# Performance work log

Measured on AMD Instinct MI355X. Metric: run time of the kernel, lower is better.

## Reference

```python
import jax, jax.numpy as jnp
import numpy as np

B, C_ENT, C_REL = 32768, 1000, 500


def setup_inputs() -> dict:
    key = jax.random.key(0)
    ks = jax.random.split(key, 6)
    return {
        "sub_input": jax.random.normal(ks[0], (B, C_ENT), dtype=jnp.float32),
        "relation_input": jax.random.normal(ks[1], (B, C_REL), dtype=jnp.float32),
        "obj_input": jax.random.normal(ks[2], (B, C_ENT), dtype=jnp.float32),
        "sub_target": jax.random.randint(ks[3], (B,), 0, C_ENT, dtype=jnp.int32),
        "relation_target": jax.random.randint(ks[4], (B,), 0, C_REL, dtype=jnp.int32),
        "obj_target": jax.random.randint(ks[5], (B,), 0, C_ENT, dtype=jnp.int32),
    }


def reference(sub_input, relation_input, obj_input, sub_target, relation_target, obj_target):
    s = jax.nn.softmax(sub_input, axis=1)
    r = jax.nn.softmax(relation_input, axis=1)
    o = jax.nn.softmax(obj_input, axis=1)
    b = s.shape[0]
    rows = jnp.arange(b)

    # ground-truth triplet probability
    gt = s[rows, sub_target] * r[rows, relation_target] * o[rows, obj_target]

    # top-2 values/indices per row (replaces full torch.sort)
    sv, si = jax.lax.top_k(s, 2)
    rv, ri = jax.lax.top_k(r, 2)
    ov, oi = jax.lax.top_k(o, 2)

    # all three argmaxes match the targets?
    cond = (si[:, 0] == sub_target) & (ri[:, 0] == relation_target) & (oi[:, 0] == obj_target)

    # 8 combinations of top-2 probs; second-smallest of the 8 (torch.sort ascending, index 1)
    tmp = (sv[:, :, None, None] * rv[:, None, :, None] * ov[:, None, None, :]).reshape(b, 8)
    second_smallest = jnp.sort(tmp, axis=1)[:, 1]

    top1 = sv[:, 0] * rv[:, 0] * ov[:, 0]
    pre = jnp.where(cond, second_smallest, top1)

    out = 1.0 - gt + pre
    return jnp.mean(jnp.maximum(out, 0.0))
```

## Files before the change

### kernel.cpp

```cpp
#include <hip/hip_runtime.h>
#include <float.h>
#include <limits.h>


constexpr int B      = 32768;
constexpr int C_ENT  = 1000;
constexpr int C_REL  = 500;


template<int NK>
__device__ inline void lane_top2(const float4* v, float& m1, float& m2) {
  float hi[2 * NK], lo[2 * NK];
#pragma unroll
  for (int k = 0; k < NK; ++k) {
    hi[2 * k]     = fmaxf(v[k].x, v[k].y);
    lo[2 * k]     = fminf(v[k].x, v[k].y);
    hi[2 * k + 1] = fmaxf(v[k].z, v[k].w);
    lo[2 * k + 1] = fminf(v[k].z, v[k].w);
  }
#pragma unroll
  for (int half = NK; half >= 1; half >>= 1) {
#pragma unroll
    for (int i = 0; i < half; ++i) {
      const float ha = hi[i], hb = hi[i + half];
      const float la = lo[i], lb = lo[i + half];
      hi[i] = fmaxf(ha, hb);
      lo[i] = fmaxf(fmaxf(la, lb), fminf(ha, hb));
    }
  }
  m1 = hi[0];
  m2 = lo[0];
}

template<int NK>
__device__ inline void lane_z_idx(const float4* v, int lane, float m1, float& z, int& idx) {
  float zp[NK];
  idx = INT_MAX;
#pragma unroll
  for (int k = 0; k < NK; ++k) {
    const int base = 4 * (lane + 64 * k);
    const float a0 = v[k].x, a1 = v[k].y, a2 = v[k].z, a3 = v[k].w;
    zp[k] = (__expf(a0 - m1) + __expf(a1 - m1)) + (__expf(a2 - m1) + __expf(a3 - m1));
    const int i01 = min(a0 == m1 ? base     : INT_MAX, a1 == m1 ? base + 1 : INT_MAX);
    const int i23 = min(a2 == m1 ? base + 2 : INT_MAX, a3 == m1 ? base + 3 : INT_MAX);
    idx = min(idx, min(i01, i23));
  }
  if constexpr (NK == 4) z = (zp[0] + zp[1]) + (zp[2] + zp[3]);
  else                   z = zp[0] + zp[1];
}

template<int NK, int C4>
__device__ inline void wave_stats2(const float* __restrict__ rowA,
                                   const float* __restrict__ rowB,
                                   int lane, int tA, int tB,
                                   float4* __restrict__ outp) {
  const float4* a4 = (const float4*)rowA;
  const float4* b4 = (const float4*)rowB;
  float4 va[NK], vb[NK];
#pragma unroll
  for (int k = 0; k < NK - 1; ++k) {
    va[k] = a4[lane + 64 * k];
    vb[k] = b4[lane + 64 * k];
  }
  {
    const int  i  = lane + 64 * (NK - 1);
    const bool ok = (i < C4);
    const int  ic = ok ? i : (C4 - 1);
    float4 ta = a4[ic], tb = b4[ic];
    ta.x = ok ? ta.x : -FLT_MAX;  ta.y = ok ? ta.y : -FLT_MAX;
    ta.z = ok ? ta.z : -FLT_MAX;  ta.w = ok ? ta.w : -FLT_MAX;
    tb.x = ok ? tb.x : -FLT_MAX;  tb.y = ok ? tb.y : -FLT_MAX;
    tb.z = ok ? tb.z : -FLT_MAX;  tb.w = ok ? tb.w : -FLT_MAX;
    va[NK - 1] = ta;
    vb[NK - 1] = tb;
  }
  const float xa = rowA[tA];
  const float xb = rowB[tB];

  float m1a, m2a, m1b, m2b;
  lane_top2<NK>(va, m1a, m2a);
  lane_top2<NK>(vb, m1b, m2b);

#pragma unroll
  for (int off = 32; off; off >>= 1) {
    const float p1a = __shfl_xor(m1a, off), p2a = __shfl_xor(m2a, off);
    const float p1b = __shfl_xor(m1b, off), p2b = __shfl_xor(m2b, off);
    m2a = fmaxf(fmaxf(m2a, p2a), fminf(m1a, p1a));
    m1a = fmaxf(m1a, p1a);
    m2b = fmaxf(fmaxf(m2b, p2b), fminf(m1b, p1b));
    m1b = fmaxf(m1b, p1b);
  }

  float za, zb;
  int   ia, ib;
  lane_z_idx<NK>(va, lane, m1a, za, ia);
  lane_z_idx<NK>(vb, lane, m1b, zb, ib);

#pragma unroll
  for (int off = 32; off; off >>= 1) {
    za += __shfl_xor(za, off);
    zb += __shfl_xor(zb, off);
    ia  = min(ia, __shfl_xor(ia, off));
    ib  = min(ib, __shfl_xor(ib, off));
  }

  if (lane == 0) {
    const float iZa = 1.0f / za;
    const float iZb = 1.0f / zb;
    outp[0] = make_float4(iZa, __expf(m2a - m1a) * iZa, __expf(xa - m1a) * iZa,
                          __int_as_float(ia));
    outp[1] = make_float4(iZb, __expf(m2b - m1b) * iZb, __expf(xb - m1b) * iZb,
                          __int_as_float(ib));
  }
}

__global__ __launch_bounds__(256) void stats2_kernel(
    const float* __restrict__ s, const float* __restrict__ r, const float* __restrict__ o,
    const int* __restrict__ st, const int* __restrict__ rt, const int* __restrict__ ot,
    float4* __restrict__ out4) {
  const int wid  = threadIdx.x >> 6;
  const int lane = threadIdx.x & 63;
  const int gw   = blockIdx.x * 4 + wid;
  const int m    = gw >> 14;
  const int p    = gw & 16383;
  const int row  = 2 * p;
  if (m == 0)
    wave_stats2<4, C_ENT / 4>(s + (size_t)row * C_ENT, s + (size_t)(row + 1) * C_ENT,
                              lane, st[row], st[row + 1], out4 + row);
  else if (m == 1)
    wave_stats2<4, C_ENT / 4>(o + (size_t)row * C_ENT, o + (size_t)(row + 1) * C_ENT,
                              lane, ot[row], ot[row + 1], out4 + B + row);
  else
    wave_stats2<2, C_REL / 4>(r + (size_t)row * C_REL, r + (size_t)(row + 1) * C_REL,
                              lane, rt[row], rt[row + 1], out4 + 2 * B + row);
}

__global__ __launch_bounds__(256) void combine_kernel(
    const float4* __restrict__ stat4,
    const int* __restrict__ st, const int* __restrict__ rt, const int* __restrict__ ot,
    float* __restrict__ partial) {
  const int row = blockIdx.x * 256 + threadIdx.x;
  const float4 S = stat4[row];
  const float4 O = stat4[B + row];
  const float4 R = stat4[2 * B + row];
  const float gt   = S.z * R.z * O.z;
  const float top1 = S.x * R.x * O.x;
  const float c1 = S.x * R.y * O.y;
  const float c2 = S.y * R.x * O.y;
  const float c3 = S.y * R.y * O.x;
  const float second = fminf(c1, fminf(c2, c3));
  const bool cond = (__float_as_int(S.w) == st[row]) &&
                    (__float_as_int(R.w) == rt[row]) &&
                    (__float_as_int(O.w) == ot[row]);
  const float pre = cond ? second : top1;
  partial[row] = fmaxf(1.0f - gt + pre, 0.0f);
}


__device__ inline void combine_stats(float& m1, int& i1, float& m2, float& Z,
                                     float bm1, int bi1, float bm2, float bZ) {
  bool bwin = (bm1 > m1) || (bm1 == m1 && bi1 < i1);
  float wm1 = bwin ? bm1 : m1;
  int   wi1 = bwin ? bi1 : i1;
  float wm2 = bwin ? bm2 : m2;
  float lm1 = bwin ? m1  : bm1;
  float wZ  = bwin ? bZ  : Z;
  float lZ  = bwin ? Z   : bZ;
  m1 = wm1; i1 = wi1;
  m2 = fmaxf(wm2, lm1);
  Z  = wZ + lZ * __expf(lm1 - wm1);
}

template<int NK, int C4>
__device__ inline void row_stats(const float* __restrict__ row, int lane, int target,
                                 float& p_top1, float& p_top2, int& amax, float& p_tgt) {
  const float4* row4 = (const float4*)row;
  float4 v[NK];
#pragma unroll
  for (int k = 0; k < NK; ++k) {
    int idx = lane + 64 * k;
    v[k] = (idx < C4) ? row4[idx] : make_float4(-FLT_MAX, -FLT_MAX, -FLT_MAX, -FLT_MAX);
  }
  float m1 = -FLT_MAX, m2 = -FLT_MAX;
  int   i1 = 0x7fffffff;
#pragma unroll
  for (int k = 0; k < NK; ++k) {
    int base = 4 * (lane + 64 * k);
    float a0 = v[k].x, a1 = v[k].y, a2 = v[k].z, a3 = v[k].w;
    if (a0 > m1) { m2 = m1; m1 = a0; i1 = base;     } else if (a0 > m2) m2 = a0;
    if (a1 > m1) { m2 = m1; m1 = a1; i1 = base + 1; } else if (a1 > m2) m2 = a1;
    if (a2 > m1) { m2 = m1; m1 = a2; i1 = base + 2; } else if (a2 > m2) m2 = a2;
    if (a3 > m1) { m2 = m1; m1 = a3; i1 = base + 3; } else if (a3 > m2) m2 = a3;
  }
  float Z = 0.f;
#pragma unroll
  for (int k = 0; k < NK; ++k) {
    Z += __expf(v[k].x - m1); Z += __expf(v[k].y - m1);
    Z += __expf(v[k].z - m1); Z += __expf(v[k].w - m1);
  }
#pragma unroll
  for (int off = 32; off > 0; off >>= 1) {
    float bm1 = __shfl_xor(m1, off);
    int   bi1 = __shfl_xor(i1, off);
    float bm2 = __shfl_xor(m2, off);
    float bZ  = __shfl_xor(Z,  off);
    combine_stats(m1, i1, m2, Z, bm1, bi1, bm2, bZ);
  }
  float invZ = 1.0f / Z;
  float xt   = row[target];
  p_top1 = invZ;
  p_top2 = __expf(m2 - m1) * invZ;
  p_tgt  = __expf(xt - m1) * invZ;
  amax   = i1;
}

template<bool ATOMIC>
__global__ __launch_bounds__(256) void rank_loss_kernel(
    const float* __restrict__ s, const float* __restrict__ r, const float* __restrict__ o,
    const int* __restrict__ st, const int* __restrict__ rt, const int* __restrict__ ot,
    float* __restrict__ partial, float* __restrict__ out) {
  const int wid  = threadIdx.x >> 6;
  const int lane = threadIdx.x & 63;
  const int row  = blockIdx.x * 4 + wid;

  const float* srow = s + (size_t)row * C_ENT;
  const float* rrow = r + (size_t)row * C_REL;
  const float* orow = o + (size_t)row * C_ENT;
  const int tS = st[row], tR = rt[row], tO = ot[row];

  float sp0, sp1, spt; int sa;
  float rp0, rp1, rpt; int ra;
  float op0, op1, opt; int oa;
  row_stats<4, C_ENT / 4>(srow, lane, tS, sp0, sp1, sa, spt);
  row_stats<2, C_REL / 4>(rrow, lane, tR, rp0, rp1, ra, rpt);
  row_stats<4, C_ENT / 4>(orow, lane, tO, op0, op1, oa, opt);

  if (lane == 0) {
    float gt   = spt * rpt * opt;
    float top1 = sp0 * rp0 * op0;
    float c1 = sp0 * rp1 * op1;
    float c2 = sp1 * rp0 * op1;
    float c3 = sp1 * rp1 * op0;
    float second = fminf(c1, fminf(c2, c3));
    bool cond = (sa == tS) && (ra == tR) && (oa == tO);
    float pre = cond ? second : top1;
    float val = fmaxf(1.0f - gt + pre, 0.0f);
    if (ATOMIC) atomicAdd(out, val * (1.0f / (float)B));
    else        partial[row] = val;
  }
}


__global__ __launch_bounds__(1024) void reduce_sum_kernel(const float* __restrict__ p,
                                                          float* __restrict__ out) {
  const float4* p4 = (const float4*)p;
  float sum = 0.f;
  for (int i = threadIdx.x; i < B / 4; i += 1024) {
    float4 v = p4[i];
    sum += (v.x + v.y) + (v.z + v.w);
  }
#pragma unroll
  for (int off = 32; off > 0; off >>= 1) sum += __shfl_xor(sum, off);
  __shared__ float lds[16];
  if ((threadIdx.x & 63) == 0) lds[threadIdx.x >> 6] = sum;
  __syncthreads();
  if (threadIdx.x == 0) {
    float t = 0.f;
#pragma unroll
    for (int i = 0; i < 16; ++i) t += lds[i];
    out[0] = t * (1.0f / (float)B);
  }
}

extern "C" void kernel_launch(void* const* d_in, const int* in_sizes, int n_in,
                              void* d_out, int out_size, void* d_ws, size_t ws_size,
                              hipStream_t stream) {
  const float* s  = (const float*)d_in[0];
  const float* r  = (const float*)d_in[1];
  const float* o  = (const float*)d_in[2];
  const int*   st = (const int*)d_in[3];
  const int*   rt = (const int*)d_in[4];
  const int*   ot = (const int*)d_in[5];
  float* out = (float*)d_out;

  const size_t statBytes = (size_t)3 * B * sizeof(float4);
  if (ws_size >= statBytes + (size_t)B * sizeof(float)) {
    float4* stat4  = (float4*)d_ws;
    float* partial = (float*)((char*)d_ws + statBytes);
    stats2_kernel<<<3 * B / 8, 256, 0, stream>>>(s, r, o, st, rt, ot, stat4);
    combine_kernel<<<B / 256, 256, 0, stream>>>(stat4, st, rt, ot, partial);
    reduce_sum_kernel<<<1, 1024, 0, stream>>>(partial, out);
  } else if (ws_size >= (size_t)B * sizeof(float)) {
    float* partial = (float*)d_ws;
    rank_loss_kernel<false><<<B / 4, 256, 0, stream>>>(s, r, o, st, rt, ot, partial, nullptr);
    reduce_sum_kernel<<<1, 1024, 0, stream>>>(partial, out);
  } else {
    hipMemsetAsync(d_out, 0, sizeof(float), stream);
    rank_loss_kernel<true><<<B / 4, 256, 0, stream>>>(s, r, o, st, rt, ot, nullptr, out);
  }
}
```

Before: 320.1 us.

## Fuse stats, combine and reduce into one cooperative persistent kernel with DPP reductions

Replaces the three-kernel pipeline (stats, combine, reduce) with a single cooperative persistent kernel. Waves loop over row-pair units, then a grid sync is followed by per-block loss partial sums and a second grid sync for the final reduction. Wave-level shuffle reductions in the stats path are also replaced with DPP row/bank broadcast reductions that end in lane 63. The aim is to remove two launch gaps and the per-row partial write and read, and to make the cross-lane reductions cheaper. In exchange it adds grid-wide sync cost and limits the grid to resident blocks, which could reduce latency hiding for the memory-bound stats phase.

```diff
diff --git a/kernel.cpp b/kernel.cpp
--- a/kernel.cpp
+++ b/kernel.cpp
@@ -1,11 +1,63 @@
 #include <hip/hip_runtime.h>
+#include <hip/hip_cooperative_groups.h>
 #include <float.h>
 #include <limits.h>
+
+namespace cg = cooperative_groups;
 
 
 constexpr int B      = 32768;
 constexpr int C_ENT  = 1000;
 constexpr int C_REL  = 500;
+constexpr int NUNITS = 3 * B / 2;
+
+
+template<int CTRL, int RM>
+__device__ inline float fdpp(float x, float ident) {
+  return __int_as_float(__builtin_amdgcn_update_dpp(
+      __float_as_int(ident), __float_as_int(x), CTRL, RM, 0xF, false));
+}
+template<int CTRL, int RM>
+__device__ inline int idpp(int x, int ident) {
+  return __builtin_amdgcn_update_dpp(ident, x, CTRL, RM, 0xF, false);
+}
+__device__ inline float readlane63(float x) {
+  return __int_as_float(__builtin_amdgcn_readlane(__float_as_int(x), 63));
+}
+
+template<int CTRL, int RM>
+__device__ inline void top2_stage(float& m1, float& m2) {
+  const float q1 = fdpp<CTRL, RM>(m1, -FLT_MAX);
+  const float q2 = fdpp<CTRL, RM>(m2, -FLT_MAX);
+  m2 = fmaxf(fmaxf(m2, q2), fminf(m1, q1));
+  m1 = fmaxf(m1, q1);
+}
+__device__ inline void top2_reduce63(float& m1, float& m2) {
+  top2_stage<0xB1,  0xF>(m1, m2);
+  top2_stage<0x4E,  0xF>(m1, m2);
+  top2_stage<0x141, 0xF>(m1, m2);
+  top2_stage<0x140, 0xF>(m1, m2);
+  top2_stage<0x142, 0xA>(m1, m2);
+  top2_stage<0x143, 0xC>(m1, m2);
+}
+__device__ inline float sum_reduce63(float z) {
+  z += fdpp<0xB1,  0xF>(z, 0.f);
+  z += fdpp<0x4E,  0xF>(z, 0.f);
+  z += fdpp<0x141, 0xF>(z, 0.f);
+  z += fdpp<0x140, 0xF>(z, 0.f);
+  z += fdpp<0x142, 0xA>(z, 0.f);
+  z += fdpp<0x143, 0xC>(z, 0.f);
+  return z;
+}
+__device__ inline int min_reduce63(int v) {
+  v = min(v, idpp<0xB1,  0xF>(v, INT_MAX));
+  v = min(v, idpp<0x4E,  0xF>(v, INT_MAX));
+  v = min(v, idpp<0x141, 0xF>(v, INT_MAX));
+  v = min(v, idpp<0x140, 0xF>(v, INT_MAX));
+  v = min(v, idpp<0x142, 0xA>(v, INT_MAX));
+  v = min(v, idpp<0x143, 0xC>(v, INT_MAX));
+  return v;
+}
 
 
 template<int NK>
@@ -80,31 +132,21 @@
   float m1a, m2a, m1b, m2b;
   lane_top2<NK>(va, m1a, m2a);
   lane_top2<NK>(vb, m1b, m2b);
-
-#pragma unroll
-  for (int off = 32; off; off >>= 1) {
-    const float p1a = __shfl_xor(m1a, off), p2a = __shfl_xor(m2a, off);
-    const float p1b = __shfl_xor(m1b, off), p2b = __shfl_xor(m2b, off);
-    m2a = fmaxf(fmaxf(m2a, p2a), fminf(m1a, p1a));
-    m1a = fmaxf(m1a, p1a);
-    m2b = fmaxf(fmaxf(m2b, p2b), fminf(m1b, p1b));
-    m1b = fmaxf(m1b, p1b);
-  }
+  top2_reduce63(m1a, m2a);
+  top2_reduce63(m1b, m2b);
+  m1a = readlane63(m1a);  m2a = readlane63(m2a);
+  m1b = readlane63(m1b);  m2b = readlane63(m2b);
 
   float za, zb;
   int   ia, ib;
   lane_z_idx<NK>(va, lane, m1a, za, ia);
   lane_z_idx<NK>(vb, lane, m1b, zb, ib);
-
-#pragma unroll
-  for (int off = 32; off; off >>= 1) {
-    za += __shfl_xor(za, off);
-    zb += __shfl_xor(zb, off);
-    ia  = min(ia, __shfl_xor(ia, off));
-    ib  = min(ib, __shfl_xor(ib, off));
-  }
-
-  if (lane == 0) {
+  za = sum_reduce63(za);
+  zb = sum_reduce63(zb);
+  ia = min_reduce63(ia);
+  ib = min_reduce63(ib);
+
+  if (lane == 63) {
     const float iZa = 1.0f / za;
     const float iZb = 1.0f / zb;
     outp[0] = make_float4(iZa, __expf(m2a - m1a) * iZa, __expf(xa - m1a) * iZa,
@@ -114,32 +156,25 @@
   }
 }
 
-__global__ __launch_bounds__(256) void stats2_kernel(
+__device__ inline void do_unit(int gw,
     const float* __restrict__ s, const float* __restrict__ r, const float* __restrict__ o,
     const int* __restrict__ st, const int* __restrict__ rt, const int* __restrict__ ot,
-    float4* __restrict__ out4) {
-  const int wid  = threadIdx.x >> 6;
-  const int lane = threadIdx.x & 63;
-  const int gw   = blockIdx.x * 4 + wid;
-  const int m    = gw >> 14;
-  const int p    = gw & 16383;
-  const int row  = 2 * p;
+    float4* __restrict__ stat4, int lane) {
+  const int m   = gw >> 14;
+  const int row = (gw & 16383) * 2;
   if (m == 0)
     wave_stats2<4, C_ENT / 4>(s + (size_t)row * C_ENT, s + (size_t)(row + 1) * C_ENT,
-                              lane, st[row], st[row + 1], out4 + row);
+                              lane, st[row], st[row + 1], stat4 + row);
   else if (m == 1)
     wave_stats2<4, C_ENT / 4>(o + (size_t)row * C_ENT, o + (size_t)(row + 1) * C_ENT,
-                              lane, ot[row], ot[row + 1], out4 + B + row);
+                              lane, ot[row], ot[row + 1], stat4 + B + row);
   else
     wave_stats2<2, C_REL / 4>(r + (size_t)row * C_REL, r + (size_t)(row + 1) * C_REL,
-                              lane, rt[row], rt[row + 1], out4 + 2 * B + row);
-}
-
-__global__ __launch_bounds__(256) void combine_kernel(
-    const float4* __restrict__ stat4,
-    const int* __restrict__ st, const int* __restrict__ rt, const int* __restrict__ ot,
-    float* __restrict__ partial) {
-  const int row = blockIdx.x * 256 + threadIdx.x;
+                              lane, rt[row], rt[row + 1], stat4 + 2 * B + row);
+}
+
+__device__ inline float row_loss(const float4* __restrict__ stat4, int row,
+                                 int ts, int tr, int to) {
   const float4 S = stat4[row];
   const float4 O = stat4[B + row];
   const float4 R = stat4[2 * B + row];
@@ -149,11 +184,87 @@
   const float c2 = S.y * R.x * O.y;
   const float c3 = S.y * R.y * O.x;
   const float second = fminf(c1, fminf(c2, c3));
-  const bool cond = (__float_as_int(S.w) == st[row]) &&
-                    (__float_as_int(R.w) == rt[row]) &&
-                    (__float_as_int(O.w) == ot[row]);
+  const bool cond = (__float_as_int(S.w) == ts) &&
+                    (__float_as_int(R.w) == tr) &&
+                    (__float_as_int(O.w) == to);
   const float pre = cond ? second : top1;
-  partial[row] = fmaxf(1.0f - gt + pre, 0.0f);
+  return fmaxf(1.0f - gt + pre, 0.0f);
+}
+
+
+__global__ __launch_bounds__(256, 8) void fused_kernel(
+    const float* __restrict__ s, const float* __restrict__ r, const float* __restrict__ o,
+    const int* __restrict__ st, const int* __restrict__ rt, const int* __restrict__ ot,
+    float4* __restrict__ stat4, float* __restrict__ partial, float* __restrict__ out) {
+  const int wid  = threadIdx.x >> 6;
+  const int lane = threadIdx.x & 63;
+  const int nslots = gridDim.x * 4;
+  for (int gw = blockIdx.x * 4 + wid; gw < NUNITS; gw += nslots)
+    do_unit(gw, s, r, o, st, rt, ot, stat4, lane);
+
+  cg::this_grid().sync();
+
+  float sum = 0.f;
+  for (int row = blockIdx.x * 256 + threadIdx.x; row < B; row += gridDim.x * 256)
+    sum += row_loss(stat4, row, st[row], rt[row], ot[row]);
+#pragma unroll
+  for (int off = 32; off; off >>= 1) sum += __shfl_xor(sum, off);
+  __shared__ float lds[4];
+  if (lane == 0) lds[wid] = sum;
+  __syncthreads();
+  if (threadIdx.x == 0) partial[blockIdx.x] = (lds[0] + lds[1]) + (lds[2] + lds[3]);
+
+  cg::this_grid().sync();
+
+  if (blockIdx.x == 0) {
+    float t = 0.f;
+    for (int i = threadIdx.x; i < (int)gridDim.x; i += 256) t += partial[i];
+#pragma unroll
+    for (int off = 32; off; off >>= 1) t += __shfl_xor(t, off);
+    if (lane == 0) lds[wid] = t;
+    __syncthreads();
+    if (threadIdx.x == 0)
+      out[0] = ((lds[0] + lds[1]) + (lds[2] + lds[3])) * (1.0f / (float)B);
+  }
+}
+
+
+__global__ __launch_bounds__(256) void stats2_kernel(
+    const float* __restrict__ s, const float* __restrict__ r, const float* __restrict__ o,
+    const int* __restrict__ st, const int* __restrict__ rt, const int* __restrict__ ot,
+    float4* __restrict__ out4) {
+  const int wid  = threadIdx.x >> 6;
+  const int lane = threadIdx.x & 63;
+  do_unit(blockIdx.x * 4 + wid, s, r, o, st, rt, ot, out4, lane);
+}
+
+__global__ __launch_bounds__(256) void combine_kernel(
+    const float4* __restrict__ stat4,
+    const int* __restrict__ st, const int* __restrict__ rt, const int* __restrict__ ot,
+    float* __restrict__ partial) {
+  const int row = blockIdx.x * 256 + threadIdx.x;
+  partial[row] = row_loss(stat4, row, st[row], rt[row], ot[row]);
+}
+
+__global__ __launch_bounds__(1024) void reduce_sum_kernel(const float* __restrict__ p,
+                                                          float* __restrict__ out) {
+  const float4* p4 = (const float4*)p;
+  float sum = 0.f;
+  for (int i = threadIdx.x; i < B / 4; i += 1024) {
+    float4 v = p4[i];
+    sum += (v.x + v.y) + (v.z + v.w);
+  }
+#pragma unroll
+  for (int off = 32; off > 0; off >>= 1) sum += __shfl_xor(sum, off);
+  __shared__ float lds[16];
+  if ((threadIdx.x & 63) == 0) lds[threadIdx.x >> 6] = sum;
+  __syncthreads();
+  if (threadIdx.x == 0) {
+    float t = 0.f;
+#pragma unroll
+    for (int i = 0; i < 16; ++i) t += lds[i];
+    out[0] = t * (1.0f / (float)B);
+  }
 }
 
 
@@ -214,26 +325,21 @@
   amax   = i1;
 }
 
-template<bool ATOMIC>
 __global__ __launch_bounds__(256) void rank_loss_kernel(
     const float* __restrict__ s, const float* __restrict__ r, const float* __restrict__ o,
     const int* __restrict__ st, const int* __restrict__ rt, const int* __restrict__ ot,
-    float* __restrict__ partial, float* __restrict__ out) {
+    float* __restrict__ out) {
   const int wid  = threadIdx.x >> 6;
   const int lane = threadIdx.x & 63;
   const int row  = blockIdx.x * 4 + wid;
 
-  const float* srow = s + (size_t)row * C_ENT;
-  const float* rrow = r + (size_t)row * C_REL;
-  const float* orow = o + (size_t)row * C_ENT;
   const int tS = st[row], tR = rt[row], tO = ot[row];
-
   float sp0, sp1, spt; int sa;
   float rp0, rp1, rpt; int ra;
   float op0, op1, opt; int oa;
-  row_stats<4, C_ENT / 4>(srow, lane, tS, sp0, sp1, sa, spt);
-  row_stats<2, C_REL / 4>(rrow, lane, tR, rp0, rp1, ra, rpt);
-  row_stats<4, C_ENT / 4>(orow, lane, tO, op0, op1, oa, opt);
+  row_stats<4, C_ENT / 4>(s + (size_t)row * C_ENT, lane, tS, sp0, sp1, sa, spt);
+  row_stats<2, C_REL / 4>(r + (size_t)row * C_REL, lane, tR, rp0, rp1, ra, rpt);
+  row_stats<4, C_ENT / 4>(o + (size_t)row * C_ENT, lane, tO, op0, op1, oa, opt);
 
   if (lane == 0) {
     float gt   = spt * rpt * opt;
@@ -244,33 +350,10 @@
     float second = fminf(c1, fminf(c2, c3));
     bool cond = (sa == tS) && (ra == tR) && (oa == tO);
     float pre = cond ? second : top1;
-    float val = fmaxf(1.0f - gt + pre, 0.0f);
-    if (ATOMIC) atomicAdd(out, val * (1.0f / (float)B));
-    else        partial[row] = val;
-  }
-}
-
-
-__global__ __launch_bounds__(1024) void reduce_sum_kernel(const float* __restrict__ p,
-                                                          float* __restrict__ out) {
-  const float4* p4 = (const float4*)p;
-  float sum = 0.f;
-  for (int i = threadIdx.x; i < B / 4; i += 1024) {
-    float4 v = p4[i];
-    sum += (v.x + v.y) + (v.z + v.w);
-  }
-#pragma unroll
-  for (int off = 32; off > 0; off >>= 1) sum += __shfl_xor(sum, off);
-  __shared__ float lds[16];
-  if ((threadIdx.x & 63) == 0) lds[threadIdx.x >> 6] = sum;
-  __syncthreads();
-  if (threadIdx.x == 0) {
-    float t = 0.f;
-#pragma unroll
-    for (int i = 0; i < 16; ++i) t += lds[i];
-    out[0] = t * (1.0f / (float)B);
-  }
-}
+    atomicAdd(out, fmaxf(1.0f - gt + pre, 0.0f) * (1.0f / (float)B));
+  }
+}
+
 
 extern "C" void kernel_launch(void* const* d_in, const int* in_sizes, int n_in,
                               void* d_out, int out_size, void* d_ws, size_t ws_size,
@@ -283,19 +366,40 @@
   const int*   ot = (const int*)d_in[5];
   float* out = (float*)d_out;
 
+  static int coopBlocks = -2;
+  if (coopBlocks == -2) {
+    int dev = 0;
+    hipGetDevice(&dev);
+    int coop = 0;
+    hipDeviceGetAttribute(&coop, hipDeviceAttributeCooperativeLaunch, dev);
+    if (coop) {
+      int bpc = 0;
+      hipError_t e = hipOccupancyMaxActiveBlocksPerMultiprocessor(&bpc, fused_kernel, 256, 0);
+      hipDeviceProp_t prop;
+      hipGetDeviceProperties(&prop, dev);
+      coopBlocks = (e == hipSuccess && bpc > 0)
+                       ? min(bpc * prop.multiProcessorCount, 2048) : -1;
+    } else {
+      coopBlocks = -1;
+    }
+  }
+
   const size_t statBytes = (size_t)3 * B * sizeof(float4);
   if (ws_size >= statBytes + (size_t)B * sizeof(float)) {
     float4* stat4  = (float4*)d_ws;
     float* partial = (float*)((char*)d_ws + statBytes);
-    stats2_kernel<<<3 * B / 8, 256, 0, stream>>>(s, r, o, st, rt, ot, stat4);
-    combine_kernel<<<B / 256, 256, 0, stream>>>(stat4, st, rt, ot, partial);
-    reduce_sum_kernel<<<1, 1024, 0, stream>>>(partial, out);
-  } else if (ws_size >= (size_t)B * sizeof(float)) {
-    float* partial = (float*)d_ws;
-    rank_loss_kernel<false><<<B / 4, 256, 0, stream>>>(s, r, o, st, rt, ot, partial, nullptr);
-    reduce_sum_kernel<<<1, 1024, 0, stream>>>(partial, out);
+    if (coopBlocks > 0) {
+      void* args[] = {(void*)&s, (void*)&r, (void*)&o, (void*)&st, (void*)&rt,
+                      (void*)&ot, (void*)&stat4, (void*)&partial, (void*)&out};
+      hipLaunchCooperativeKernel(fused_kernel, dim3(coopBlocks), dim3(256),
+                                 args, 0, stream);
+    } else {
+      stats2_kernel<<<NUNITS / 4, 256, 0, stream>>>(s, r, o, st, rt, ot, stat4);
+      combine_kernel<<<B / 256, 256, 0, stream>>>(stat4, st, rt, ot, partial);
+      reduce_sum_kernel<<<1, 1024, 0, stream>>>(partial, out);
+    }
   } else {
     hipMemsetAsync(d_out, 0, sizeof(float), stream);
-    rank_loss_kernel<true><<<B / 4, 256, 0, stream>>>(s, r, o, st, rt, ot, nullptr, out);
-  }
-}
+    rank_loss_kernel<<<B / 4, 256, 0, stream>>>(s, r, o, st, rt, ot, out);
+  }
+}
```

After: 459.1 us. 43.4% more time.

## Fuse combine and reduction into stats kernel via last-block counter

Applied to the files above, without the earlier changes.

Replaces the three-launch stats/combine/reduce pipeline with a single stats kernel in which the last block to finish, detected through an atomic counter, computes every per-row loss and the final mean. This removes two kernel launches and the partial-buffer round trip. In exchange a single 256-thread block processes all 32768 rows serially at the tail, and a memset is added to reset the counter.

```diff
diff --git a/kernel.cpp b/kernel.cpp
--- a/kernel.cpp
+++ b/kernel.cpp
@@ -6,6 +6,7 @@
 constexpr int B      = 32768;
 constexpr int C_ENT  = 1000;
 constexpr int C_REL  = 500;
+constexpr int NUNITS = 3 * B / 2;
 
 
 template<int NK>
@@ -114,32 +115,25 @@
   }
 }
 
-__global__ __launch_bounds__(256) void stats2_kernel(
+__device__ inline void do_unit(int gw,
     const float* __restrict__ s, const float* __restrict__ r, const float* __restrict__ o,
     const int* __restrict__ st, const int* __restrict__ rt, const int* __restrict__ ot,
-    float4* __restrict__ out4) {
-  const int wid  = threadIdx.x >> 6;
-  const int lane = threadIdx.x & 63;
-  const int gw   = blockIdx.x * 4 + wid;
-  const int m    = gw >> 14;
-  const int p    = gw & 16383;
-  const int row  = 2 * p;
+    float4* __restrict__ stat4, int lane) {
+  const int m   = gw >> 14;
+  const int row = (gw & 16383) * 2;
   if (m == 0)
     wave_stats2<4, C_ENT / 4>(s + (size_t)row * C_ENT, s + (size_t)(row + 1) * C_ENT,
-                              lane, st[row], st[row + 1], out4 + row);
+                              lane, st[row], st[row + 1], stat4 + row);
   else if (m == 1)
     wave_stats2<4, C_ENT / 4>(o + (size_t)row * C_ENT, o + (size_t)(row + 1) * C_ENT,
-                              lane, ot[row], ot[row + 1], out4 + B + row);
+                              lane, ot[row], ot[row + 1], stat4 + B + row);
   else
     wave_stats2<2, C_REL / 4>(r + (size_t)row * C_REL, r + (size_t)(row + 1) * C_REL,
-                              lane, rt[row], rt[row + 1], out4 + 2 * B + row);
-}
-
-__global__ __launch_bounds__(256) void combine_kernel(
-    const float4* __restrict__ stat4,
-    const int* __restrict__ st, const int* __restrict__ rt, const int* __restrict__ ot,
-    float* __restrict__ partial) {
-  const int row = blockIdx.x * 256 + threadIdx.x;
+                              lane, rt[row], rt[row + 1], stat4 + 2 * B + row);
+}
+
+__device__ inline float row_loss(const float4* __restrict__ stat4, int row,
+                                 int ts, int tr, int to) {
   const float4 S = stat4[row];
   const float4 O = stat4[B + row];
   const float4 R = stat4[2 * B + row];
@@ -149,11 +143,43 @@
   const float c2 = S.y * R.x * O.y;
   const float c3 = S.y * R.y * O.x;
   const float second = fminf(c1, fminf(c2, c3));
-  const bool cond = (__float_as_int(S.w) == st[row]) &&
-                    (__float_as_int(R.w) == rt[row]) &&
-                    (__float_as_int(O.w) == ot[row]);
+  const bool cond = (__float_as_int(S.w) == ts) &&
+                    (__float_as_int(R.w) == tr) &&
+                    (__float_as_int(O.w) == to);
   const float pre = cond ? second : top1;
-  partial[row] = fmaxf(1.0f - gt + pre, 0.0f);
+  return fmaxf(1.0f - gt + pre, 0.0f);
+}
+
+
+__global__ __launch_bounds__(256) void stats_finish_kernel(
+    const float* __restrict__ s, const float* __restrict__ r, const float* __restrict__ o,
+    const int* __restrict__ st, const int* __restrict__ rt, const int* __restrict__ ot,
+    float4* __restrict__ stat4, unsigned* __restrict__ counter,
+    float* __restrict__ out) {
+  const int wid  = threadIdx.x >> 6;
+  const int lane = threadIdx.x & 63;
+  do_unit(blockIdx.x * 4 + wid, s, r, o, st, rt, ot, stat4, lane);
+
+  __shared__ unsigned isLast;
+  __syncthreads();
+  if (threadIdx.x == 0) {
+    __threadfence();
+    isLast = (atomicAdd(counter, 1u) == (unsigned)(gridDim.x - 1));
+  }
+  __syncthreads();
+  if (!isLast) return;
+
+  __threadfence();
+  float sum = 0.f;
+  for (int row = threadIdx.x; row < B; row += 256)
+    sum += row_loss(stat4, row, st[row], rt[row], ot[row]);
+#pragma unroll
+  for (int off = 32; off; off >>= 1) sum += __shfl_xor(sum, off);
+  __shared__ float lds[4];
+  if (lane == 0) lds[wid] = sum;
+  __syncthreads();
+  if (threadIdx.x == 0)
+    out[0] = ((lds[0] + lds[1]) + (lds[2] + lds[3])) * (1.0f / (float)B);
 }
 
 
@@ -214,26 +240,21 @@
   amax   = i1;
 }
 
-template<bool ATOMIC>
 __global__ __launch_bounds__(256) void rank_loss_kernel(
     const float* __restrict__ s, const float* __restrict__ r, const float* __restrict__ o,
     const int* __restrict__ st, const int* __restrict__ rt, const int* __restrict__ ot,
-    float* __restrict__ partial, float* __restrict__ out) {
+    float* __restrict__ out) {
   const int wid  = threadIdx.x >> 6;
   const int lane = threadIdx.x & 63;
   const int row  = blockIdx.x * 4 + wid;
 
-  const float* srow = s + (size_t)row * C_ENT;
-  const float* rrow = r + (size_t)row * C_REL;
-  const float* orow = o + (size_t)row * C_ENT;
   const int tS = st[row], tR = rt[row], tO = ot[row];
-
   float sp0, sp1, spt; int sa;
   float rp0, rp1, rpt; int ra;
   float op0, op1, opt; int oa;
-  row_stats<4, C_ENT / 4>(srow, lane, tS, sp0, sp1, sa, spt);
-  row_stats<2, C_REL / 4>(rrow, lane, tR, rp0, rp1, ra, rpt);
-  row_stats<4, C_ENT / 4>(orow, lane, tO, op0, op1, oa, opt);
+  row_stats<4, C_ENT / 4>(s + (size_t)row * C_ENT, lane, tS, sp0, sp1, sa, spt);
+  row_stats<2, C_REL / 4>(r + (size_t)row * C_REL, lane, tR, rp0, rp1, ra, rpt);
+  row_stats<4, C_ENT / 4>(o + (size_t)row * C_ENT, lane, tO, op0, op1, oa, opt);
 
   if (lane == 0) {
     float gt   = spt * rpt * opt;
@@ -244,33 +265,10 @@
     float second = fminf(c1, fminf(c2, c3));
     bool cond = (sa == tS) && (ra == tR) && (oa == tO);
     float pre = cond ? second : top1;
-    float val = fmaxf(1.0f - gt + pre, 0.0f);
-    if (ATOMIC) atomicAdd(out, val * (1.0f / (float)B));
-    else        partial[row] = val;
-  }
-}
-
-
-__global__ __launch_bounds__(1024) void reduce_sum_kernel(const float* __restrict__ p,
-                                                          float* __restrict__ out) {
-  const float4* p4 = (const float4*)p;
-  float sum = 0.f;
-  for (int i = threadIdx.x; i < B / 4; i += 1024) {
-    float4 v = p4[i];
-    sum += (v.x + v.y) + (v.z + v.w);
-  }
-#pragma unroll
-  for (int off = 32; off > 0; off >>= 1) sum += __shfl_xor(sum, off);
-  __shared__ float lds[16];
-  if ((threadIdx.x & 63) == 0) lds[threadIdx.x >> 6] = sum;
-  __syncthreads();
-  if (threadIdx.x == 0) {
-    float t = 0.f;
-#pragma unroll
-    for (int i = 0; i < 16; ++i) t += lds[i];
-    out[0] = t * (1.0f / (float)B);
-  }
-}
+    atomicAdd(out, fmaxf(1.0f - gt + pre, 0.0f) * (1.0f / (float)B));
+  }
+}
+
 
 extern "C" void kernel_launch(void* const* d_in, const int* in_sizes, int n_in,
                               void* d_out, int out_size, void* d_ws, size_t ws_size,
@@ -284,18 +282,14 @@
   float* out = (float*)d_out;
 
   const size_t statBytes = (size_t)3 * B * sizeof(float4);
-  if (ws_size >= statBytes + (size_t)B * sizeof(float)) {
-    float4* stat4  = (float4*)d_ws;
-    float* partial = (float*)((char*)d_ws + statBytes);
-    stats2_kernel<<<3 * B / 8, 256, 0, stream>>>(s, r, o, st, rt, ot, stat4);
-    combine_kernel<<<B / 256, 256, 0, stream>>>(stat4, st, rt, ot, partial);
-    reduce_sum_kernel<<<1, 1024, 0, stream>>>(partial, out);
-  } else if (ws_size >= (size_t)B * sizeof(float)) {
-    float* partial = (float*)d_ws;
-    rank_loss_kernel<false><<<B / 4, 256, 0, stream>>>(s, r, o, st, rt, ot, partial, nullptr);
-    reduce_sum_kernel<<<1, 1024, 0, stream>>>(partial, out);
+  if (ws_size >= statBytes + sizeof(unsigned)) {
+    float4*   stat4   = (float4*)d_ws;
+    unsigned* counter = (unsigned*)((char*)d_ws + statBytes);
+    hipMemsetAsync(counter, 0, sizeof(unsigned), stream);
+    stats_finish_kernel<<<NUNITS / 4, 256, 0, stream>>>(s, r, o, st, rt, ot,
+                                                        stat4, counter, out);
   } else {
     hipMemsetAsync(d_out, 0, sizeof(float), stream);
-    rank_loss_kernel<true><<<B / 4, 256, 0, stream>>>(s, r, o, st, rt, ot, nullptr, out);
-  }
-}
+    rank_loss_kernel<<<B / 4, 256, 0, stream>>>(s, r, o, st, rt, ot, out);
+  }
+}
```

Result: slower. 930.7 us (+190.8%).
